# Performance work log

Measured on AMD Instinct MI355X. Metric: run time of the kernel, lower is better.

Reference implementation:

```python
import jax, jax.numpy as jnp
import numpy as np

N = 8192      # n_nodes (graphs[0].shape[0])
E = 262144    # n_edges (avg degree 32)
B = 16        # batch
T = 15        # time taps H of ChebTimeConv
K = 25        # Chebyshev order
G1, G2 = 32, 64
C, D = 512, 6


def setup_inputs() -> dict:
    key = jax.random.key(0)
    ks = jax.random.split(key, 8)
    x = jax.random.normal(ks[0], (B, N, T), jnp.float32)
    edge_index = jax.random.randint(ks[1], (2, E), 0, N, dtype=jnp.int64)
    # ChebTimeConv weights: K Chebyshev taps x T time taps (f_in=1) -> G1
    W1 = jax.random.normal(ks[2], (K, T, G1), jnp.float32) * 0.05
    b1 = jnp.zeros((G1,), jnp.float32)
    # ChebConv weights: K taps, G1 -> G2
    W2 = jax.random.normal(ks[3], (K, G1, G2), jnp.float32) * 0.05
    b2 = jnp.zeros((G2,), jnp.float32)
    fc1_w = jax.random.normal(ks[4], (C, N * G2), jnp.float32) * 0.01
    fc1_b = jnp.zeros((C,), jnp.float32)
    fc2_w = jax.random.normal(ks[5], (D, C), jnp.float32) * 0.05
    fc2_b = jnp.zeros((D,), jnp.float32)
    return dict(x=x, edge_index=edge_index, W1=W1, b1=b1, W2=W2, b2=b2,
                fc1_w=fc1_w, fc1_b=fc1_b, fc2_w=fc2_w, fc2_b=fc2_b)


def _cheb_edge_norm(edge_index, n):
    # PyG ChebConv normalization with lambda_max=2:
    # L_hat = 2L/lambda_max - I = -D^{-1/2} A D^{-1/2} (diag cancels to 0)
    row, col = edge_index[0], edge_index[1]
    deg = jnp.zeros((n,), jnp.float32).at[row].add(1.0)
    dinv = jnp.where(deg > 0, jax.lax.rsqrt(jnp.maximum(deg, 1.0)), 0.0)
    return -(dinv[row] * dinv[col])


def _cheb_conv(x, edge_index, W, b):
    # x: [B, N, Fin]; W: [K, Fin, Fout] -> [B, N, Fout]
    row, col = edge_index[0], edge_index[1]
    norm = _cheb_edge_norm(edge_index, x.shape[1])

    def Lhat(z):  # sparse L_hat @ z : gather at source row, scatter-add at col
        msg = z[:, row, :] * norm[None, :, None]
        return jnp.zeros_like(z).at[:, col, :].add(msg)

    Tx0 = x
    out = jnp.einsum('bnf,fg->bng', Tx0, W[0])
    Tx1 = Lhat(x)
    out = out + jnp.einsum('bnf,fg->bng', Tx1, W[1])
    for k in range(2, W.shape[0]):  # fixed small K=25 recursion
        Tx2 = 2.0 * Lhat(Tx1) - Tx0
        out = out + jnp.einsum('bnf,fg->bng', Tx2, W[k])
        Tx0, Tx1 = Tx1, Tx2
    return out + b


def reference(x, edge_index, W1, b1, W2, b2, fc1_w, fc1_b, fc2_w, fc2_b):
    # torch: real part of FFT over the time axis
    xf = jnp.fft.fft(x, axis=2).real.astype(x.dtype)          # [B, N, T]
    h = jax.nn.relu(_cheb_conv(xf, edge_index, W1, b1))       # [B, N, G1]
    h = jax.nn.relu(_cheb_conv(h, edge_index, W2, b2))        # [B, N, G2]
    h = h.reshape(h.shape[0], -1)                             # [B, N*G2]
    h = h @ fc1_w.T + fc1_b                                   # [B, C]
    h = h @ fc2_w.T + fc2_b                                   # [B, D]
    return jax.nn.log_softmax(h, axis=1)
```

## Files before the change

kernel.cpp:

```cpp
#include <hip/hip_runtime.h>
#include <hip/hip_bf16.h>

typedef _Float16 f16x2 __attribute__((ext_vector_type(2)));
typedef _Float16 f16x4 __attribute__((ext_vector_type(4)));
typedef _Float16 f16x8 __attribute__((ext_vector_type(8)));
typedef float f32x4 __attribute__((ext_vector_type(4)));

static constexpr int NNODE = 8192;
static constexpr int NEDGE = 262144;
static constexpr int NBATCH = 16;
static constexpr int TDIM = 15;
static constexpr int G1D = 32;
static constexpr int G2D = 64;
static constexpr int NK = 25;
static constexpr size_t NG2 = (size_t)NNODE * G2D;
static constexpr size_t SROW = 64;
static constexpr size_t SLICE = (size_t)NNODE * SROW;


__global__ void deg_cnt_kernel(const int* __restrict__ ei, int* __restrict__ deg,
                               int* __restrict__ cnt) {
    int e = blockIdx.x * 256 + threadIdx.x;
    if (e < NEDGE) {
        atomicAdd(&deg[ei[e]], 1);
        atomicAdd(&cnt[ei[NEDGE + e]], 1);
    }
}

__global__ void dinv_kernel(const int* __restrict__ deg, float* __restrict__ dinv) {
    int n = blockIdx.x * 256 + threadIdx.x;
    if (n < NNODE) dinv[n] = (deg[n] > 0) ? rsqrtf((float)deg[n]) : 0.f;
}

__global__ __launch_bounds__(1024) void scan_kernel(const int* __restrict__ cnt,
                                                    int* __restrict__ ptr) {
    __shared__ int s[1024];
    int t = threadIdx.x;
    int base = t * 8;
    int loc[8];
    int sum = 0;
#pragma unroll
    for (int i = 0; i < 8; ++i) { loc[i] = sum; sum += cnt[base + i]; }
    s[t] = sum;
    __syncthreads();
    for (int off = 1; off < 1024; off <<= 1) {
        int v = (t >= off) ? s[t - off] : 0;
        __syncthreads();
        s[t] += v;
        __syncthreads();
    }
    int prev = (t > 0) ? s[t - 1] : 0;
#pragma unroll
    for (int i = 0; i < 8; ++i) ptr[base + i] = prev + loc[i];
    if (t == 1023) ptr[NNODE] = s[1023];
}

__global__ void fill_kernel(const int* __restrict__ ei, const int* __restrict__ ptr,
                            int* __restrict__ fill, const float* __restrict__ dinv,
                            unsigned int* __restrict__ pack) {
    int e = blockIdx.x * 256 + threadIdx.x;
    if (e < NEDGE) {
        int r = ei[e], c = ei[NEDGE + e];
        int pos = ptr[c] + atomicAdd(&fill[c], 1);
        _Float16 h = (_Float16)(-dinv[r] * dinv[c]);
        unsigned short wb = *reinterpret_cast<unsigned short*>(&h);
        pack[pos] = ((unsigned int)r << 16) | wb;
    }
}


__global__ __launch_bounds__(256) void fft_kernel(const float* __restrict__ x,
                                                  _Float16* __restrict__ T0) {
    int n = blockIdx.x;
    __shared__ float xl[NBATCH][TDIM];
    __shared__ float ct[TDIM][TDIM];
    int t = threadIdx.x;
    if (t < NBATCH * TDIM) {
        int b = t / TDIM, s = t % TDIM;
        xl[b][s] = x[((size_t)b * NNODE + n) * TDIM + s];
    }
    if (t < TDIM * TDIM) {
        int tt = t / TDIM, s = t % TDIM;
        ct[tt][s] = cosf(6.283185307179586f * (float)((tt * s) % TDIM) / 15.0f);
    }
    __syncthreads();
    int b = t >> 4, f = t & 15;
    float a = 0.f;
    if (f < TDIM) {
#pragma unroll
        for (int s = 0; s < TDIM; ++s) a += xl[b][s] * ct[f][s];
    }
    T0[((size_t)(b >> 3) * NNODE + n) * 128 + (b & 7) * 16 + f] = (_Float16)a;
}


__global__ void wt_kernel(const float* __restrict__ W, _Float16* __restrict__ Wt,
                          int F, int G, int total) {
    int i = blockIdx.x * 256 + threadIdx.x;
    if (i < total) {
        int f = i & 31;
        int g = (i >> 5) % G;
        int k = i / (32 * G);
        float v = (f < F) ? W[((size_t)k * F + f) * G + g] : 0.f;
        Wt[i] = (_Float16)v;
    }
}


template <int Q, bool FIRST>
__global__ __launch_bounds__(256, 8) void gather_step(
    const f16x2* __restrict__ Tsrc, const f16x2* __restrict__ Tprev0,
    f16x2* __restrict__ Tdst, const int* __restrict__ cptr,
    const unsigned int* __restrict__ pack) {
    constexpr int CH = 8 / Q;
    const int bid = blockIdx.x;
    const int xcd = bid & 7;
    const int s = xcd / CH;
    const int chunk = xcd % CH;
    const int wv = threadIdx.x >> 6, lane = threadIdx.x & 63;
    const int node = (chunk * (256 * Q) + (bid >> 3)) * 4 + wv;

    const f16x2* __restrict__ src = Tsrc + (size_t)s * SLICE;
    float a0 = 0.f, a1 = 0.f;
    const int p0 = cptr[node], p1 = cptr[node + 1];
    for (int tb = p0; tb < p1; tb += 64) {
        int m = p1 - tb;
        if (m > 64) m = 64;
        unsigned int pk = (lane < m) ? pack[tb + lane] : 0u;
        int j = 0;
        for (; j + 8 <= m; j += 8) {
            unsigned int q[8];
            f16x2 r[8];
#pragma unroll
            for (int u = 0; u < 8; ++u) q[u] = __builtin_amdgcn_readlane(pk, j + u);
#pragma unroll
            for (int u = 0; u < 8; ++u) r[u] = src[(size_t)(q[u] >> 16) * SROW + lane];
#pragma unroll
            for (int u = 0; u < 8; ++u) {
                unsigned short hb = (unsigned short)q[u];
                float w = (float)*reinterpret_cast<_Float16*>(&hb);
                a0 += w * (float)r[u][0];
                a1 += w * (float)r[u][1];
            }
        }
        for (; j < m; ++j) {
            unsigned int q = __builtin_amdgcn_readlane(pk, j);
            unsigned short hb = (unsigned short)q;
            float w = (float)*reinterpret_cast<_Float16*>(&hb);
            f16x2 r = src[(size_t)(q >> 16) * SROW + lane];
            a0 += w * (float)r[0];
            a1 += w * (float)r[1];
        }
    }

    f16x2 o;
    if (FIRST) {
        o[0] = (_Float16)a0; o[1] = (_Float16)a1;
    } else {
        f16x2 t0 = __builtin_nontemporal_load(
            &(Tprev0 + (size_t)s * SLICE)[(size_t)node * SROW + lane]);
        o[0] = (_Float16)(2.f * a0 - (float)t0[0]);
        o[1] = (_Float16)(2.f * a1 - (float)t0[1]);
    }
    __builtin_nontemporal_store(o, &(Tdst + (size_t)s * SLICE)[(size_t)node * SROW + lane]);
}


__global__ __launch_bounds__(128) void proj1_kernel(
    const unsigned int* __restrict__ Tall, const _Float16* __restrict__ Wt,
    const float* __restrict__ bias, _Float16* __restrict__ dest) {
    constexpr int STRIDE = NK * 32 + 8;
    __shared__ _Float16 A[16 * STRIDE];
    unsigned int* Adw = reinterpret_cast<unsigned int*>(A);
    const int n = blockIdx.x;
    const int tid = threadIdx.x;

    for (int i = tid; i < 16 * STRIDE / 2; i += 128) Adw[i] = 0u;
    __syncthreads();
    for (int idx = tid; idx < NK * 128; idx += 128) {
        int k = idx >> 7, r = idx & 127;
        int h = r >> 6, j = r & 63;
        int bl = j >> 3, jp = j & 7;
        int b = h * 8 + bl;
        Adw[b * (STRIDE / 2) + k * 16 + jp] =
            __builtin_nontemporal_load(&Tall[((size_t)(k * 2 + h) * NNODE + n) * 64 + j]);
    }
    __syncthreads();

    const int wv = tid >> 6, lane = tid & 63;
    const int m0 = lane & 15;
    const int krow = lane >> 4;
    const int k0 = krow * 8;
    const int g = wv * 16 + m0;
    const float bb = bias[g];
    f32x4 d = (f32x4){bb, bb, bb, bb};
#pragma unroll
    for (int k = 0; k < NK; ++k) {
        f16x8 af = *reinterpret_cast<const f16x8*>(&A[m0 * STRIDE + k * 32 + k0]);
        f16x8 bf = *reinterpret_cast<const f16x8*>(&Wt[((size_t)k * G1D + g) * 32 + k0]);
        d = __builtin_amdgcn_mfma_f32_16x16x32_f16(af, bf, d, 0, 0, 0);
    }
#pragma unroll
    for (int r = 0; r < 4; ++r) {
        int b = krow * 4 + r;
        _Float16 v = (_Float16)fmaxf(d[r], 0.f);
        dest[((size_t)(b >> 2) * NNODE + n) * 128 + (b & 3) * 32 + g] = v;
    }
}


__global__ __launch_bounds__(256) void proj2_kernel(
    const unsigned int* __restrict__ Tall, const _Float16* __restrict__ Wt,
    const float* __restrict__ bias, _Float16* __restrict__ dest) {
    constexpr int STRIDE = NK * 32 + 8;
    __shared__ _Float16 A[16 * STRIDE];
    unsigned int* Adw = reinterpret_cast<unsigned int*>(A);
    const int n = blockIdx.x;
    const int tid = threadIdx.x;

    for (int i = tid; i < 16 * STRIDE / 2; i += 256) Adw[i] = 0u;
    __syncthreads();
    for (int idx = tid; idx < NK * 256; idx += 256) {
        int k = idx >> 8, r = idx & 255;
        int q = r >> 6, j = r & 63;
        int bl2 = j >> 4, jp = j & 15;
        int b = q * 4 + bl2;
        Adw[b * (STRIDE / 2) + k * 16 + jp] =
            __builtin_nontemporal_load(&Tall[((size_t)(k * 4 + q) * NNODE + n) * 64 + j]);
    }
    __syncthreads();

    const int wv = tid >> 6, lane = tid & 63;
    const int m0 = lane & 15;
    const int krow = lane >> 4;
    const int k0 = krow * 8;
    const int g = wv * 16 + m0;
    const float bb = bias[g];
    f32x4 d = (f32x4){bb, bb, bb, bb};
#pragma unroll
    for (int k = 0; k < NK; ++k) {
        f16x8 af = *reinterpret_cast<const f16x8*>(&A[m0 * STRIDE + k * 32 + k0]);
        f16x8 bf = *reinterpret_cast<const f16x8*>(&Wt[((size_t)k * G2D + g) * 32 + k0]);
        d = __builtin_amdgcn_mfma_f32_16x16x32_f16(af, bf, d, 0, 0, 0);
    }
#pragma unroll
    for (int r = 0; r < 4; ++r) {
        int b = krow * 4 + r;
        _Float16 v = (_Float16)fmaxf(d[r], 0.f);
        dest[(size_t)b * NG2 + (size_t)n * G2D + g] = v;
    }
}


__global__ __launch_bounds__(512) void fc1_kernel(const _Float16* __restrict__ Hflat,
                                                  const float* __restrict__ fc1w,
                                                  float* __restrict__ partial) {
    int wave = threadIdx.x >> 6, lane = threadIdx.x & 63;
    int chunk = blockIdx.x & 127, cg = blockIdx.x >> 7;
    int c0 = (cg * 8 + wave) * 8;
    const float* wp = fc1w + (size_t)c0 * NG2 + (size_t)chunk * 4096;
    const _Float16* h = Hflat + (size_t)chunk * 4096;
    float acc[8][16];
#pragma unroll
    for (int c = 0; c < 8; ++c)
#pragma unroll
        for (int b = 0; b < 16; ++b) acc[c][b] = 0.f;

    for (int it = 0; it < 16; ++it) {
        int j = it * 256 + lane * 4;
        f32x4 wv8[8];
#pragma unroll
        for (int c = 0; c < 8; ++c)
            wv8[c] = __builtin_nontemporal_load(
                reinterpret_cast<const f32x4*>(wp + (size_t)c * NG2 + j));
#pragma unroll
        for (int b = 0; b < 16; ++b) {
            f16x4 hv = *reinterpret_cast<const f16x4*>(h + (size_t)b * NG2 + j);
            float h0 = (float)hv[0], h1 = (float)hv[1];
            float h2 = (float)hv[2], h3 = (float)hv[3];
#pragma unroll
            for (int c = 0; c < 8; ++c)
                acc[c][b] += wv8[c][0] * h0 + wv8[c][1] * h1 + wv8[c][2] * h2 + wv8[c][3] * h3;
        }
    }
#pragma unroll
    for (int c = 0; c < 8; ++c)
#pragma unroll
        for (int b = 0; b < 16; ++b) {
            float v = acc[c][b];
            for (int off = 32; off; off >>= 1) v += __shfl_down(v, off);
            if (lane == 0) partial[((size_t)chunk * 512 + c0 + c) * 16 + b] = v;
        }
}

__global__ void fc1_reduce_kernel(const float* __restrict__ partial,
                                  const float* __restrict__ fc1b, float* __restrict__ h1) {
    int i = blockIdx.x * 256 + threadIdx.x;
    if (i < 512 * 16) {
        int b = i & 15, c = i >> 4;
        float s = fc1b[c];
        for (int ch = 0; ch < 128; ++ch) s += partial[((size_t)ch * 512 + c) * 16 + b];
        h1[b * 512 + c] = s;
    }
}

__global__ __launch_bounds__(1024) void fc2_kernel(const float* __restrict__ h1,
                                                   const float* __restrict__ fc2w,
                                                   const float* __restrict__ fc2b,
                                                   float* __restrict__ out) {
    __shared__ float z[16][8];
    int wave = threadIdx.x >> 6, lane = threadIdx.x & 63;
    for (int d = 0; d < 6; ++d) {
        float acc = 0.f;
        for (int c = lane; c < 512; c += 64) acc += h1[wave * 512 + c] * fc2w[d * 512 + c];
        for (int off = 32; off; off >>= 1) acc += __shfl_down(acc, off);
        if (lane == 0) z[wave][d] = acc + fc2b[d];
    }
    __syncthreads();
    int t = threadIdx.x;
    if (t < 96) {
        int b = t / 6, d = t % 6;
        float m = z[b][0];
#pragma unroll
        for (int j = 1; j < 6; ++j) m = fmaxf(m, z[b][j]);
        float se = 0.f;
#pragma unroll
        for (int j = 0; j < 6; ++j) se += expf(z[b][j] - m);
        out[b * 6 + d] = z[b][d] - m - logf(se);
    }
}


extern "C" void kernel_launch(void* const* d_in, const int* in_sizes, int n_in,
                              void* d_out, int out_size, void* d_ws, size_t ws_size,
                              hipStream_t stream) {
    const float* x = (const float*)d_in[0];
    const int* ei = (const int*)d_in[1];
    const float* W1 = (const float*)d_in[2];
    const float* b1 = (const float*)d_in[3];
    const float* W2 = (const float*)d_in[4];
    const float* b2 = (const float*)d_in[5];
    const float* fc1w = (const float*)d_in[6];
    const float* fc1b = (const float*)d_in[7];
    const float* fc2w = (const float*)d_in[8];
    const float* fc2b = (const float*)d_in[9];
    float* out = (float*)d_out;

    char* ws = (char*)d_ws;
    size_t o = 0;
    auto alloc = [&](size_t bytes) -> void* {
        void* p = ws + o;
        o += (bytes + 255) & ~(size_t)255;
        return p;
    };
    f16x2* Tall1 = (f16x2*)alloc(NK * 2 * SLICE * 4);
    f16x2* Tall2 = (f16x2*)alloc(NK * 4 * SLICE * 4);
    _Float16* Hflat = (_Float16*)alloc(NBATCH * NG2 * 2);
    float* partial = (float*)alloc((size_t)128 * 512 * 16 * 4);
    int* deg = (int*)alloc(3 * NNODE * 4);
    int* cnt = deg + NNODE;
    int* fill = cnt + NNODE;
    int* cptr = (int*)alloc((NNODE + 8) * 4);
    float* dinv = (float*)alloc(NNODE * 4);
    unsigned int* pack = (unsigned int*)alloc((size_t)NEDGE * 4);
    _Float16* Wt1 = (_Float16*)alloc(NK * G1D * 32 * 2);
    _Float16* Wt2 = (_Float16*)alloc(NK * G2D * 32 * 2);
    float* h1 = (float*)alloc(16 * 512 * 4);

    hipMemsetAsync(deg, 0, 3 * NNODE * 4, stream);
    deg_cnt_kernel<<<NEDGE / 256, 256, 0, stream>>>(ei, deg, cnt);
    dinv_kernel<<<NNODE / 256, 256, 0, stream>>>(deg, dinv);
    scan_kernel<<<1, 1024, 0, stream>>>(cnt, cptr);
    fill_kernel<<<NEDGE / 256, 256, 0, stream>>>(ei, cptr, fill, dinv, pack);
    fft_kernel<<<NNODE, 256, 0, stream>>>(x, (_Float16*)Tall1);
    wt_kernel<<<(NK * G1D * 32 + 255) / 256, 256, 0, stream>>>(W1, Wt1, 15, G1D,
                                                               NK * G1D * 32);
    wt_kernel<<<(NK * G2D * 32 + 255) / 256, 256, 0, stream>>>(W2, Wt2, 32, G2D,
                                                               NK * G2D * 32);

    gather_step<2, true><<<4096, 256, 0, stream>>>(Tall1, nullptr, Tall1 + 2 * SLICE,
                                                   cptr, pack);
    for (int k = 2; k < NK; ++k) {
        gather_step<2, false><<<4096, 256, 0, stream>>>(
            Tall1 + (size_t)(k - 1) * 2 * SLICE, Tall1 + (size_t)(k - 2) * 2 * SLICE,
            Tall1 + (size_t)k * 2 * SLICE, cptr, pack);
    }
    proj1_kernel<<<NNODE, 128, 0, stream>>>((const unsigned int*)Tall1, Wt1, b1,
                                            (_Float16*)Tall2);

    gather_step<4, true><<<8192, 256, 0, stream>>>(Tall2, nullptr, Tall2 + 4 * SLICE,
                                                   cptr, pack);
    for (int k = 2; k < NK; ++k) {
        gather_step<4, false><<<8192, 256, 0, stream>>>(
            Tall2 + (size_t)(k - 1) * 4 * SLICE, Tall2 + (size_t)(k - 2) * 4 * SLICE,
            Tall2 + (size_t)k * 4 * SLICE, cptr, pack);
    }
    proj2_kernel<<<NNODE, 256, 0, stream>>>((const unsigned int*)Tall2, Wt2, b2, Hflat);

    fc1_kernel<<<128 * 8, 512, 0, stream>>>(Hflat, fc1w, partial);
    fc1_reduce_kernel<<<32, 256, 0, stream>>>(partial, fc1b, h1);
    fc2_kernel<<<1, 1024, 0, stream>>>(h1, fc2w, fc2b, out);
}
```

Baseline: 1.485 ms.

## Store full node feature rows contiguously and gather wide vectors per lane

Replaces the sliced layout, where features were split into 256-byte slices per XCD-mapped block with f16x2 per lane, with one contiguous row per node: 512 bytes for layer 1 and 1 KB for layer 2. Each lane now loads an f16x4 or f16x8 vector per edge, so each neighbour's row is read once rather than once per slice. Fewer blocks are launched, and the XCD-aware slice assignment that kept each slice resident in one L2 is dropped. The intent is fewer gather instructions and fewer index reads, in exchange for a larger per-XCD L2 working set and more registers per thread.

Result: slower. 1.656 ms (+11.6%).

```diff
diff --git a/kernel.cpp b/kernel.cpp
--- a/kernel.cpp
+++ b/kernel.cpp
@@ -14,8 +14,8 @@
 static constexpr int G2D = 64;
 static constexpr int NK = 25;
 static constexpr size_t NG2 = (size_t)NNODE * G2D;
-static constexpr size_t SROW = 64;
-static constexpr size_t SLICE = (size_t)NNODE * SROW;
+static constexpr size_t S1 = (size_t)NNODE * 256;
+static constexpr size_t S2 = (size_t)NNODE * 512;
 
 
 __global__ void deg_cnt_kernel(const int* __restrict__ ei, int* __restrict__ deg,
@@ -90,7 +90,7 @@
 #pragma unroll
         for (int s = 0; s < TDIM; ++s) a += xl[b][s] * ct[f][s];
     }
-    T0[((size_t)(b >> 3) * NNODE + n) * 128 + (b & 7) * 16 + f] = (_Float16)a;
+    T0[(size_t)n * 256 + t] = (_Float16)a;
 }
 
 
@@ -107,21 +107,20 @@
 }
 
 
-template <int Q, bool FIRST>
+template <int VL, bool FIRST>
 __global__ __launch_bounds__(256, 8) void gather_step(
-    const f16x2* __restrict__ Tsrc, const f16x2* __restrict__ Tprev0,
-    f16x2* __restrict__ Tdst, const int* __restrict__ cptr,
+    const _Float16* __restrict__ Tsrc, const _Float16* __restrict__ Tprev0,
+    _Float16* __restrict__ Tdst, const int* __restrict__ cptr,
     const unsigned int* __restrict__ pack) {
-    constexpr int CH = 8 / Q;
-    const int bid = blockIdx.x;
-    const int xcd = bid & 7;
-    const int s = xcd / CH;
-    const int chunk = xcd % CH;
+    typedef _Float16 vec_t __attribute__((ext_vector_type(VL)));
     const int wv = threadIdx.x >> 6, lane = threadIdx.x & 63;
-    const int node = (chunk * (256 * Q) + (bid >> 3)) * 4 + wv;
-
-    const f16x2* __restrict__ src = Tsrc + (size_t)s * SLICE;
-    float a0 = 0.f, a1 = 0.f;
+    const int node = blockIdx.x * 4 + wv;
+    const vec_t* __restrict__ src = reinterpret_cast<const vec_t*>(Tsrc);
+
+    float a[VL];
+#pragma unroll
+    for (int v = 0; v < VL; ++v) a[v] = 0.f;
+
     const int p0 = cptr[node], p1 = cptr[node + 1];
     for (int tb = p0; tb < p1; tb += 64) {
         int m = p1 - tb;
@@ -130,39 +129,41 @@
         int j = 0;
         for (; j + 8 <= m; j += 8) {
             unsigned int q[8];
-            f16x2 r[8];
+            vec_t r[8];
 #pragma unroll
             for (int u = 0; u < 8; ++u) q[u] = __builtin_amdgcn_readlane(pk, j + u);
 #pragma unroll
-            for (int u = 0; u < 8; ++u) r[u] = src[(size_t)(q[u] >> 16) * SROW + lane];
+            for (int u = 0; u < 8; ++u) r[u] = src[(size_t)(q[u] >> 16) * 64 + lane];
 #pragma unroll
             for (int u = 0; u < 8; ++u) {
                 unsigned short hb = (unsigned short)q[u];
                 float w = (float)*reinterpret_cast<_Float16*>(&hb);
-                a0 += w * (float)r[u][0];
-                a1 += w * (float)r[u][1];
+#pragma unroll
+                for (int v = 0; v < VL; ++v) a[v] += w * (float)r[u][v];
             }
         }
         for (; j < m; ++j) {
             unsigned int q = __builtin_amdgcn_readlane(pk, j);
             unsigned short hb = (unsigned short)q;
             float w = (float)*reinterpret_cast<_Float16*>(&hb);
-            f16x2 r = src[(size_t)(q >> 16) * SROW + lane];
-            a0 += w * (float)r[0];
-            a1 += w * (float)r[1];
+            vec_t r = src[(size_t)(q >> 16) * 64 + lane];
+#pragma unroll
+            for (int v = 0; v < VL; ++v) a[v] += w * (float)r[v];
         }
     }
 
-    f16x2 o;
+    vec_t o;
     if (FIRST) {
-        o[0] = (_Float16)a0; o[1] = (_Float16)a1;
+#pragma unroll
+        for (int v = 0; v < VL; ++v) o[v] = (_Float16)a[v];
     } else {
-        f16x2 t0 = __builtin_nontemporal_load(
-            &(Tprev0 + (size_t)s * SLICE)[(size_t)node * SROW + lane]);
-        o[0] = (_Float16)(2.f * a0 - (float)t0[0]);
-        o[1] = (_Float16)(2.f * a1 - (float)t0[1]);
-    }
-    __builtin_nontemporal_store(o, &(Tdst + (size_t)s * SLICE)[(size_t)node * SROW + lane]);
+        vec_t t0 = __builtin_nontemporal_load(
+            reinterpret_cast<const vec_t*>(Tprev0) + (size_t)node * 64 + lane);
+#pragma unroll
+        for (int v = 0; v < VL; ++v) o[v] = (_Float16)(2.f * a[v] - (float)t0[v]);
+    }
+    __builtin_nontemporal_store(
+        o, reinterpret_cast<vec_t*>(Tdst) + (size_t)node * 64 + lane);
 }
 
 
@@ -178,12 +179,10 @@
     for (int i = tid; i < 16 * STRIDE / 2; i += 128) Adw[i] = 0u;
     __syncthreads();
     for (int idx = tid; idx < NK * 128; idx += 128) {
-        int k = idx >> 7, r = idx & 127;
-        int h = r >> 6, j = r & 63;
-        int bl = j >> 3, jp = j & 7;
-        int b = h * 8 + bl;
+        int k = idx >> 7, j = idx & 127;
+        int b = j >> 3, jp = j & 7;
         Adw[b * (STRIDE / 2) + k * 16 + jp] =
-            __builtin_nontemporal_load(&Tall[((size_t)(k * 2 + h) * NNODE + n) * 64 + j]);
+            __builtin_nontemporal_load(&Tall[((size_t)k * NNODE + n) * 128 + j]);
     }
     __syncthreads();
 
@@ -204,7 +203,7 @@
     for (int r = 0; r < 4; ++r) {
         int b = krow * 4 + r;
         _Float16 v = (_Float16)fmaxf(d[r], 0.f);
-        dest[((size_t)(b >> 2) * NNODE + n) * 128 + (b & 3) * 32 + g] = v;
+        dest[(size_t)n * 512 + b * 32 + g] = v;
     }
 }
 
@@ -221,12 +220,10 @@
     for (int i = tid; i < 16 * STRIDE / 2; i += 256) Adw[i] = 0u;
     __syncthreads();
     for (int idx = tid; idx < NK * 256; idx += 256) {
-        int k = idx >> 8, r = idx & 255;
-        int q = r >> 6, j = r & 63;
-        int bl2 = j >> 4, jp = j & 15;
-        int b = q * 4 + bl2;
+        int k = idx >> 8, j = idx & 255;
+        int b = j >> 4, jp = j & 15;
         Adw[b * (STRIDE / 2) + k * 16 + jp] =
-            __builtin_nontemporal_load(&Tall[((size_t)(k * 4 + q) * NNODE + n) * 64 + j]);
+            __builtin_nontemporal_load(&Tall[((size_t)k * NNODE + n) * 256 + j]);
     }
     __syncthreads();
 
@@ -353,8 +350,8 @@
         o += (bytes + 255) & ~(size_t)255;
         return p;
     };
-    f16x2* Tall1 = (f16x2*)alloc(NK * 2 * SLICE * 4);
-    f16x2* Tall2 = (f16x2*)alloc(NK * 4 * SLICE * 4);
+    _Float16* Tall1 = (_Float16*)alloc(NK * S1 * 2);
+    _Float16* Tall2 = (_Float16*)alloc(NK * S2 * 2);
     _Float16* Hflat = (_Float16*)alloc(NBATCH * NG2 * 2);
     float* partial = (float*)alloc((size_t)128 * 512 * 16 * 4);
     int* deg = (int*)alloc(3 * NNODE * 4);
@@ -372,28 +369,27 @@
     dinv_kernel<<<NNODE / 256, 256, 0, stream>>>(deg, dinv);
     scan_kernel<<<1, 1024, 0, stream>>>(cnt, cptr);
     fill_kernel<<<NEDGE / 256, 256, 0, stream>>>(ei, cptr, fill, dinv, pack);
-    fft_kernel<<<NNODE, 256, 0, stream>>>(x, (_Float16*)Tall1);
+    fft_kernel<<<NNODE, 256, 0, stream>>>(x, Tall1);
     wt_kernel<<<(NK * G1D * 32 + 255) / 256, 256, 0, stream>>>(W1, Wt1, 15, G1D,
                                                                NK * G1D * 32);
     wt_kernel<<<(NK * G2D * 32 + 255) / 256, 256, 0, stream>>>(W2, Wt2, 32, G2D,
                                                                NK * G2D * 32);
 
-    gather_step<2, true><<<4096, 256, 0, stream>>>(Tall1, nullptr, Tall1 + 2 * SLICE,
-                                                   cptr, pack);
+    gather_step<4, true><<<NNODE / 4, 256, 0, stream>>>(Tall1, nullptr, Tall1 + S1,
+                                                        cptr, pack);
     for (int k = 2; k < NK; ++k) {
-        gather_step<2, false><<<4096, 256, 0, stream>>>(
-            Tall1 + (size_t)(k - 1) * 2 * SLICE, Tall1 + (size_t)(k - 2) * 2 * SLICE,
-            Tall1 + (size_t)k * 2 * SLICE, cptr, pack);
-    }
-    proj1_kernel<<<NNODE, 128, 0, stream>>>((const unsigned int*)Tall1, Wt1, b1,
-                                            (_Float16*)Tall2);
-
-    gather_step<4, true><<<8192, 256, 0, stream>>>(Tall2, nullptr, Tall2 + 4 * SLICE,
-                                                   cptr, pack);
+        gather_step<4, false><<<NNODE / 4, 256, 0, stream>>>(
+            Tall1 + (size_t)(k - 1) * S1, Tall1 + (size_t)(k - 2) * S1,
+            Tall1 + (size_t)k * S1, cptr, pack);
+    }
+    proj1_kernel<<<NNODE, 128, 0, stream>>>((const unsigned int*)Tall1, Wt1, b1, Tall2);
+
+    gather_step<8, true><<<NNODE / 4, 256, 0, stream>>>(Tall2, nullptr, Tall2 + S2,
+                                                        cptr, pack);
     for (int k = 2; k < NK; ++k) {
-        gather_step<4, false><<<8192, 256, 0, stream>>>(
-            Tall2 + (size_t)(k - 1) * 4 * SLICE, Tall2 + (size_t)(k - 2) * 4 * SLICE,
-            Tall2 + (size_t)k * 4 * SLICE, cptr, pack);
+        gather_step<8, false><<<NNODE / 4, 256, 0, stream>>>(
+            Tall2 + (size_t)(k - 1) * S2, Tall2 + (size_t)(k - 2) * S2,
+            Tall2 + (size_t)k * S2, cptr, pack);
     }
     proj2_kernel<<<NNODE, 256, 0, stream>>>((const unsigned int*)Tall2, Wt2, b2, Hflat);
 
```

## Loop over slices per wave with XCD-staggered phase instead of XCD-partitioned slices

Applied to the files above, without the earlier changes.

The gather kernel used to give each XCD a fixed slice so that slice stayed resident in that XCD's L2. Now each wave handles all Q slices for its node, one after another, starting at a slice offset taken from the hardware XCC_ID register, and the grid shrinks to NNODE/4 blocks. This removes the static block-to-XCD mapping assumption and reuses the CSR pointer and edge-pack reads across slices. The cost is that every XCD now touches all slices, so L2 locality may suffer, and each wave does Q times more serial work.

Result: slower. 1.665 ms (+12.1%).

```diff
diff --git a/kernel.cpp b/kernel.cpp
--- a/kernel.cpp
+++ b/kernel.cpp
@@ -108,61 +108,63 @@
 
 
 template <int Q, bool FIRST>
-__global__ __launch_bounds__(256, 8) void gather_step(
+__global__ __launch_bounds__(256, 8) void gather_phased(
     const f16x2* __restrict__ Tsrc, const f16x2* __restrict__ Tprev0,
     f16x2* __restrict__ Tdst, const int* __restrict__ cptr,
     const unsigned int* __restrict__ pack) {
-    constexpr int CH = 8 / Q;
-    const int bid = blockIdx.x;
-    const int xcd = bid & 7;
-    const int s = xcd / CH;
-    const int chunk = xcd % CH;
     const int wv = threadIdx.x >> 6, lane = threadIdx.x & 63;
-    const int node = (chunk * (256 * Q) + (bid >> 3)) * 4 + wv;
-
-    const f16x2* __restrict__ src = Tsrc + (size_t)s * SLICE;
-    float a0 = 0.f, a1 = 0.f;
+    const int node = blockIdx.x * 4 + wv;
+    unsigned int xcc;
+    asm volatile("s_getreg_b32 %0, hwreg(HW_REG_XCC_ID)" : "=s"(xcc));
+    const int pref = (int)(((xcc & 7u) * Q) >> 3) & (Q - 1);
     const int p0 = cptr[node], p1 = cptr[node + 1];
-    for (int tb = p0; tb < p1; tb += 64) {
-        int m = p1 - tb;
-        if (m > 64) m = 64;
-        unsigned int pk = (lane < m) ? pack[tb + lane] : 0u;
-        int j = 0;
-        for (; j + 8 <= m; j += 8) {
-            unsigned int q[8];
-            f16x2 r[8];
-#pragma unroll
-            for (int u = 0; u < 8; ++u) q[u] = __builtin_amdgcn_readlane(pk, j + u);
-#pragma unroll
-            for (int u = 0; u < 8; ++u) r[u] = src[(size_t)(q[u] >> 16) * SROW + lane];
-#pragma unroll
-            for (int u = 0; u < 8; ++u) {
-                unsigned short hb = (unsigned short)q[u];
+
+    for (int p = 0; p < Q; ++p) {
+        const int s = (pref + p) & (Q - 1);
+        const f16x2* __restrict__ src = Tsrc + (size_t)s * SLICE;
+        float a0 = 0.f, a1 = 0.f;
+        for (int tb = p0; tb < p1; tb += 64) {
+            int m = p1 - tb;
+            if (m > 64) m = 64;
+            unsigned int pk = (lane < m) ? pack[tb + lane] : 0u;
+            int j = 0;
+            for (; j + 8 <= m; j += 8) {
+                unsigned int q[8];
+                f16x2 r[8];
+#pragma unroll
+                for (int u = 0; u < 8; ++u) q[u] = __builtin_amdgcn_readlane(pk, j + u);
+#pragma unroll
+                for (int u = 0; u < 8; ++u) r[u] = src[(size_t)(q[u] >> 16) * SROW + lane];
+#pragma unroll
+                for (int u = 0; u < 8; ++u) {
+                    unsigned short hb = (unsigned short)q[u];
+                    float w = (float)*reinterpret_cast<_Float16*>(&hb);
+                    a0 += w * (float)r[u][0];
+                    a1 += w * (float)r[u][1];
+                }
+            }
+            for (; j < m; ++j) {
+                unsigned int q = __builtin_amdgcn_readlane(pk, j);
+                unsigned short hb = (unsigned short)q;
                 float w = (float)*reinterpret_cast<_Float16*>(&hb);
-                a0 += w * (float)r[u][0];
-                a1 += w * (float)r[u][1];
+                f16x2 r = src[(size_t)(q >> 16) * SROW + lane];
+                a0 += w * (float)r[0];
+                a1 += w * (float)r[1];
             }
         }
-        for (; j < m; ++j) {
-            unsigned int q = __builtin_amdgcn_readlane(pk, j);
-            unsigned short hb = (unsigned short)q;
-            float w = (float)*reinterpret_cast<_Float16*>(&hb);
-            f16x2 r = src[(size_t)(q >> 16) * SROW + lane];
-            a0 += w * (float)r[0];
-            a1 += w * (float)r[1];
+
+        f16x2 o;
+        if (FIRST) {
+            o[0] = (_Float16)a0; o[1] = (_Float16)a1;
+        } else {
+            f16x2 t0 = __builtin_nontemporal_load(
+                &(Tprev0 + (size_t)s * SLICE)[(size_t)node * SROW + lane]);
+            o[0] = (_Float16)(2.f * a0 - (float)t0[0]);
+            o[1] = (_Float16)(2.f * a1 - (float)t0[1]);
         }
-    }
-
-    f16x2 o;
-    if (FIRST) {
-        o[0] = (_Float16)a0; o[1] = (_Float16)a1;
-    } else {
-        f16x2 t0 = __builtin_nontemporal_load(
-            &(Tprev0 + (size_t)s * SLICE)[(size_t)node * SROW + lane]);
-        o[0] = (_Float16)(2.f * a0 - (float)t0[0]);
-        o[1] = (_Float16)(2.f * a1 - (float)t0[1]);
-    }
-    __builtin_nontemporal_store(o, &(Tdst + (size_t)s * SLICE)[(size_t)node * SROW + lane]);
+        __builtin_nontemporal_store(
+            o, &(Tdst + (size_t)s * SLICE)[(size_t)node * SROW + lane]);
+    }
 }
 
 
@@ -378,20 +380,20 @@
     wt_kernel<<<(NK * G2D * 32 + 255) / 256, 256, 0, stream>>>(W2, Wt2, 32, G2D,
                                                                NK * G2D * 32);
 
-    gather_step<2, true><<<4096, 256, 0, stream>>>(Tall1, nullptr, Tall1 + 2 * SLICE,
-                                                   cptr, pack);
+    gather_phased<2, true><<<NNODE / 4, 256, 0, stream>>>(Tall1, nullptr,
+                                                          Tall1 + 2 * SLICE, cptr, pack);
     for (int k = 2; k < NK; ++k) {
-        gather_step<2, false><<<4096, 256, 0, stream>>>(
+        gather_phased<2, false><<<NNODE / 4, 256, 0, stream>>>(
             Tall1 + (size_t)(k - 1) * 2 * SLICE, Tall1 + (size_t)(k - 2) * 2 * SLICE,
             Tall1 + (size_t)k * 2 * SLICE, cptr, pack);
     }
     proj1_kernel<<<NNODE, 128, 0, stream>>>((const unsigned int*)Tall1, Wt1, b1,
                                             (_Float16*)Tall2);
 
-    gather_step<4, true><<<8192, 256, 0, stream>>>(Tall2, nullptr, Tall2 + 4 * SLICE,
-                                                   cptr, pack);
+    gather_phased<4, true><<<NNODE / 4, 256, 0, stream>>>(Tall2, nullptr,
+                                                          Tall2 + 4 * SLICE, cptr, pack);
     for (int k = 2; k < NK; ++k) {
-        gather_step<4, false><<<8192, 256, 0, stream>>>(
+        gather_phased<4, false><<<NNODE / 4, 256, 0, stream>>>(
             Tall2 + (size_t)(k - 1) * 4 * SLICE, Tall2 + (size_t)(k - 2) * 4 * SLICE,
             Tall2 + (size_t)k * 4 * SLICE, cptr, pack);
     }
```
